# Performance work log

Measured on AMD Instinct MI355X. Metric: run time of the kernel, lower is better.

## Reference

```python
import jax, jax.numpy as jnp
import numpy as np

GAMMA = 1.0
BIG = 1e8  # boundary value used by the original numba kernel


def setup_inputs() -> dict:
    key = jax.random.key(0)
    k1, k2 = jax.random.split(key)
    N, M, d = 4096, 4096, 64
    x = jax.random.normal(k1, (N, d), dtype=jnp.float32)
    y = jax.random.normal(k2, (M, d), dtype=jnp.float32)
    return {"x": x, "y": y}


def _soft_dtw(D, gamma):
    """Soft-DTW DP R[N,M] via anti-diagonal wavefront scan.

    Matches compute_softdtw: R padded with BIG, R[0,0]=0,
    R[i,j] = D[i-1,j-1] + softmin_gamma(R[i-1,j-1], R[i-1,j], R[i,j-1]).
    Diagonals are stored as length-(N+2) vectors indexed by i (j = k - i).
    """
    N, M = D.shape
    ii = jnp.arange(1, N + 1)          # cell row indices 1..N
    inf = jnp.full((N + 2,), BIG, D.dtype)
    r_km2 = inf.at[0].set(0.0)          # diagonal k=0: only R[0,0]=0
    r_km1 = inf                         # diagonal k=1: all boundary

    def step(carry, k):
        r_km2, r_km1 = carry
        j = k - ii                      # column index per row on this diagonal
        valid = (j >= 1) & (j <= M)
        r0 = -r_km2[ii - 1] / gamma     # R[i-1, j-1]
        r1 = -r_km1[ii - 1] / gamma     # R[i-1, j]
        r2 = -r_km1[ii] / gamma         # R[i,   j-1]
        rmax = jnp.maximum(jnp.maximum(r0, r1), r2)
        rsum = jnp.exp(r0 - rmax) + jnp.exp(r1 - rmax) + jnp.exp(r2 - rmax)
        softmin = -gamma * (jnp.log(rsum) + rmax)
        jc = jnp.clip(j - 1, 0, M - 1)
        d_diag = D[ii - 1, jc]          # D[i-1, j-1] along this diagonal
        val = jnp.where(valid, d_diag + softmin, BIG)
        r_k = inf.at[1:N + 1].set(val)
        return (r_km1, r_k), None

    ks = jnp.arange(2, N + M + 1)
    (_, r_last), _ = jax.lax.scan(step, (r_km2, r_km1), ks)
    return r_last[N]                    # R[N, M]


def reference(x, y):
    # squared-euclidean distance matrix: sum((x_i - y_j)^2)
    x2 = jnp.sum(x * x, axis=1)
    y2 = jnp.sum(y * y, axis=1)
    D = x2[:, None] + y2[None, :] - 2.0 * (x @ y.T)  # [N, M]
    N, M = D.shape
    r = _soft_dtw(D, GAMMA)
    return r / (N + M)                   # open_end=False path
```

## Files before the change

kernel.cpp:

```cpp
#include <hip/hip_runtime.h>
#include <hip/hip_fp16.h>

#define Nn 4096
#define Mm 4096
#define NB 64
#define CH 16
#define NCHUNK 260
#define NCHUNKP 262
#define HPITCH 4352
#define HOFF 64
#define LOG2E 1.4426950408889634f
#define LN2 0.6931471805599453f
#define BIGX (1 << 23)

typedef unsigned long long ull;

__device__ __forceinline__ float hw_exp2(float x) { return __builtin_amdgcn_exp2f(x); }
__device__ __forceinline__ float hw_log2(float x) { return __builtin_amdgcn_logf(x); }

__device__ __forceinline__ float dpp_shr1(float v) {
    int r = __builtin_amdgcn_update_dpp(0, __float_as_int(v), 0x138, 0xF, 0xF, false);
    return __int_as_float(r);
}
__device__ __forceinline__ int dpp_shr1_i(int v) {
    return __builtin_amdgcn_update_dpp(0, v, 0x138, 0xF, 0xF, false);
}
__device__ __forceinline__ float dpp_shl1(float v) {
    int r = __builtin_amdgcn_update_dpp(0, __float_as_int(v), 0x130, 0xF, 0xF, false);
    return __int_as_float(r);
}
__device__ __forceinline__ int dpp_shl1_i(int v) {
    return __builtin_amdgcn_update_dpp(0, v, 0x130, 0xF, 0xF, false);
}
__device__ __forceinline__ float half_lo(int w) {
    return __low2float(__builtin_bit_cast(__half2, w));
}
__device__ __forceinline__ float half_hi(int w) {
    return __high2float(__builtin_bit_cast(__half2, w));
}
__device__ __forceinline__ ull packmx(float m, int X) {
    return (ull)__float_as_uint(m) | ((ull)(unsigned)X << 32);
}

__global__ __launch_bounds__(256) void dist_kernel(const float* __restrict__ x,
                                                   const float* __restrict__ y,
                                                   __half* __restrict__ Dsk) {
    __shared__ float xs[64][65];
    __shared__ float ys[80][65];
    __shared__ float dt[64][81];
    __shared__ float x2s[64], y2s[80];
    const int b = blockIdx.y, tj = blockIdx.x, tid = threadIdx.x;

    const float4* x4 = (const float4*)(x + (size_t)b * 64 * 64);
#pragma unroll
    for (int i = 0; i < 4; ++i) {
        int idx = tid + i * 256;
        int r = idx >> 4, c = (idx & 15) * 4;
        float4 v = x4[idx];
        xs[r][c] = v.x; xs[r][c + 1] = v.y; xs[r][c + 2] = v.z; xs[r][c + 3] = v.w;
    }
#pragma unroll
    for (int i = 0; i < 5; ++i) {
        int idx = tid + i * 256;
        int r = idx >> 4, c = (idx & 15) * 4;
        int rowg = tj * 64 + r; if (rowg > Mm - 1) rowg = Mm - 1;
        float4 w = ((const float4*)(y + (size_t)rowg * 64))[c >> 2];
        ys[r][c] = w.x; ys[r][c + 1] = w.y; ys[r][c + 2] = w.z; ys[r][c + 3] = w.w;
    }
    __syncthreads();

    if (tid < 64) {
        float a = 0.f;
#pragma unroll 8
        for (int k = 0; k < 64; ++k) a += xs[tid][k] * xs[tid][k];
        x2s[tid] = a;
    } else if (tid < 144) {
        int r = tid - 64;
        float a = 0.f;
#pragma unroll 8
        for (int k = 0; k < 64; ++k) a += ys[r][k] * ys[r][k];
        y2s[r] = a;
    }
    __syncthreads();

    const int r0 = (tid >> 4) * 4, c0 = (tid & 15) * 5;
    float acc[4][5] = {{0.f}};
#pragma unroll 4
    for (int k = 0; k < 64; ++k) {
        float a0 = xs[r0][k], a1 = xs[r0 + 1][k], a2 = xs[r0 + 2][k], a3 = xs[r0 + 3][k];
#pragma unroll
        for (int j = 0; j < 5; ++j) {
            float bj = ys[c0 + j][k];
            acc[0][j] = fmaf(a0, bj, acc[0][j]);
            acc[1][j] = fmaf(a1, bj, acc[1][j]);
            acc[2][j] = fmaf(a2, bj, acc[2][j]);
            acc[3][j] = fmaf(a3, bj, acc[3][j]);
        }
    }
#pragma unroll
    for (int i = 0; i < 4; ++i)
#pragma unroll
        for (int j = 0; j < 5; ++j)
            dt[r0 + i][c0 + j] =
                (x2s[r0 + i] + y2s[c0 + j] - 2.0f * acc[i][j]) * LOG2E;
    __syncthreads();

    const int l = tid & 63, q = tid >> 6;
    const int ci = ((l + 15) >> 4) + q;
    const int jj0 = 16 * ci - l;
    int w[8];
#pragma unroll
    for (int i = 0; i < 8; ++i) {
        __half2 hh;
        hh.x = __float2half(dt[l][jj0 + 2 * i]);
        hh.y = __float2half(dt[l][jj0 + 2 * i + 1]);
        w[i] = __builtin_bit_cast(int, hh);
    }
    {
        __half* dst = Dsk + (((size_t)b * NCHUNKP + 4 * tj + ci) * 64 + l) * 16;
        int4* d4 = (int4*)dst;
        d4[0] = make_int4(w[0], w[1], w[2], w[3]);
        d4[1] = make_int4(w[4], w[5], w[6], w[7]);
    }
    if (tj == 0 && q == 0) {
        const int cif = l >> 4;
        int wf[8];
#pragma unroll
        for (int i = 0; i < 8; ++i) {
            int ja = 16 * cif - l + 2 * i;     if (ja < 0) ja = 0;
            int jb = 16 * cif - l + 2 * i + 1; if (jb < 0) jb = 0;
            __half2 hh;
            hh.x = __float2half(dt[l][ja]);
            hh.y = __float2half(dt[l][jb]);
            wf[i] = __builtin_bit_cast(int, hh);
        }
        __half* dst = Dsk + (((size_t)b * NCHUNKP + cif) * 64 + l) * 16;
        int4* d4 = (int4*)dst;
        d4[0] = make_int4(wf[0], wf[1], wf[2], wf[3]);
        d4[1] = make_int4(wf[4], wf[5], wf[6], wf[7]);
    }
}

#define PREP(KM, NI, DV) \
    float dv_##KM = (DV); float nf_##KM = __builtin_rintf(dv_##KM); \
    int NI = (int)nf_##KM; float KM = hw_exp2(nf_##KM - dv_##KM);

#define STEP(KM, NI, IDX) do {                                                \
    float shufM = dpp_shr1(lM);                                               \
    int   shufX = dpp_shr1_i(lX);                                             \
    float upM = isL0 ? hRotM : shufM;                                         \
    int   upX = isL0 ? hRotX : shufX;                                         \
    float dgM = isL0 ? hPrevM : psM;                                          \
    int   dgX = isL0 ? hPrevX : psX;                                          \
    hPrevM = hRotM; hPrevX = hRotX;                                           \
    hRotM = dpp_shl1(hRotM); hRotX = dpp_shl1_i(hRotX);                       \
    int Xm = min(min(dgX, upX), lX);                                          \
    float ssum = ldexpf(dgM, Xm - dgX) + ldexpf(upM, Xm - upX) +              \
                 ldexpf(lM, Xm - lX);                                         \
    float mraw = ssum * (KM);                                                 \
    unsigned mb = __float_as_uint(mraw);                                      \
    int e = (int)((mb >> 23) & 0xFFu) - 126;                                  \
    psM = shufM; psX = shufX;                                                 \
    lM = __uint_as_float((mb & 0x807FFFFFu) | 0x3F000000u);                   \
    lX = Xm + (NI) - e;                                                       \
    if (doStore)                                                              \
        __hip_atomic_store(&HoutB[16 * c + (IDX) - 62], packmx(lM, lX),       \
                           __ATOMIC_RELAXED, __HIP_MEMORY_SCOPE_AGENT);       \
} while (0)

__global__ __launch_bounds__(64, 1) void dp_kernel(const __half* __restrict__ Dsk,
                                                   ull* __restrict__ H,
                                                   float* __restrict__ out) {
    const int l = threadIdx.x;
    const int b = blockIdx.x;
    const bool isL0 = (l == 0), isL63 = (l == 63), lastBand = (b == NB - 1);
    const int lt = l & 15;
    const __half* __restrict__ Db = Dsk + ((size_t)b * NCHUNKP * 64 + l) * 16;
    const ull* __restrict__ HinB = H + (size_t)b * HPITCH + HOFF;
    ull* __restrict__ HoutB = H + (size_t)(b + 1) * HPITCH + HOFF;
    const bool doH = (b > 0);
    const bool doStore = (!lastBand) && isL63;

    float lM = 0.5f;  int lX = BIGX;
    float psM = 0.5f; int psX = BIGX;
    float hPrevM = 0.5f; int hPrevX = (b == 0) ? -1 : BIGX;
    float hRotM; int hRotX;
    ull hNextU, hLoadU;
    int4 dn1A, dn1B, dn2A, dn2B;
    float rTM = 0.5f; int rTX = 0;

    {
        const int4* p = (const int4*)Db;
        dn1A = p[0]; dn1B = p[1];
        const int4* q = (const int4*)(Db + 1024);
        dn2A = q[0]; dn2B = q[1];
    }
    if (doH) {
        hNextU = __hip_atomic_load(&HinB[1 + lt],      __ATOMIC_RELAXED, __HIP_MEMORY_SCOPE_AGENT);
        hLoadU = __hip_atomic_load(&HinB[CH + 1 + lt], __ATOMIC_RELAXED, __HIP_MEMORY_SCOPE_AGENT);
    } else {
        hNextU = packmx(0.5f, BIGX);
        hLoadU = packmx(0.5f, BIGX);
    }

    for (int c = 0; c < NCHUNK; ++c) {
        int4 dcA = dn1A, dcB = dn1B;
        dn1A = dn2A; dn1B = dn2B;
        {
            const int4* p = (const int4*)(Db + (size_t)(c + 2) * 1024);
            dn2A = p[0]; dn2B = p[1];
        }
        hRotM = __uint_as_float((unsigned)hNextU);
        hRotX = (int)(unsigned)(hNextU >> 32);
        hNextU = hLoadU;
        if (doH && (c + 2 <= 255))
            hLoadU = __hip_atomic_load(&HinB[16 * (c + 2) + 1 + lt],
                                       __ATOMIC_RELAXED, __HIP_MEMORY_SCOPE_AGENT);
        if (doH && (c <= 255)) {
            while (__ballot(!(hRotM > 0.f))) {
                __builtin_amdgcn_s_sleep(1);
                ull v = __hip_atomic_load(&HinB[16 * c + 1 + lt],
                                          __ATOMIC_RELAXED, __HIP_MEMORY_SCOPE_AGENT);
                hRotM = __uint_as_float((unsigned)v);
                hRotX = (int)(unsigned)(v >> 32);
            }
        }

        PREP(k0,  n0,  half_lo(dcA.x)); PREP(k1,  n1,  half_hi(dcA.x));
        PREP(k2,  n2,  half_lo(dcA.y)); PREP(k3,  n3,  half_hi(dcA.y));
        PREP(k4,  n4,  half_lo(dcA.z)); PREP(k5,  n5,  half_hi(dcA.z));
        PREP(k6,  n6,  half_lo(dcA.w)); PREP(k7,  n7,  half_hi(dcA.w));
        PREP(k8,  n8,  half_lo(dcB.x)); PREP(k9,  n9,  half_hi(dcB.x));
        PREP(k10, n10, half_lo(dcB.y)); PREP(k11, n11, half_hi(dcB.y));
        PREP(k12, n12, half_lo(dcB.z)); PREP(k13, n13, half_hi(dcB.z));
        PREP(k14, n14, half_lo(dcB.w)); PREP(k15, n15, half_hi(dcB.w));

        STEP(k0,  n0,  0);  STEP(k1,  n1,  1);  STEP(k2,  n2,  2);
        STEP(k3,  n3,  3);  STEP(k4,  n4,  4);  STEP(k5,  n5,  5);
        STEP(k6,  n6,  6);  STEP(k7,  n7,  7);  STEP(k8,  n8,  8);
        STEP(k9,  n9,  9);  STEP(k10, n10, 10); STEP(k11, n11, 11);
        STEP(k12, n12, 12); STEP(k13, n13, 13); STEP(k14, n14, 14);
        if (c == NCHUNK - 1) { rTM = lM; rTX = lX; }
        STEP(k15, n15, 15);
    }

    if (lastBand && isL63) {
        float rpr = (float)rTX - hw_log2(rTM);
        out[0] = rpr * (LN2 / (float)(Nn + Mm));
    }
}

extern "C" void kernel_launch(void* const* d_in, const int* in_sizes, int n_in,
                              void* d_out, int out_size, void* d_ws, size_t ws_size,
                              hipStream_t stream) {
    const float* x = (const float*)d_in[0];
    const float* y = (const float*)d_in[1];
    float* out = (float*)d_out;

    char* ws = (char*)d_ws;
    __half* Dsk = (__half*)ws;
    size_t dskBytes = (size_t)NB * NCHUNKP * 64 * 16 * sizeof(__half);
    ull* H = (ull*)(ws + dskBytes);

    dist_kernel<<<dim3(64, 64), 256, 0, stream>>>(x, y, Dsk);
    dp_kernel<<<NB, 64, 0, stream>>>(Dsk, H, out);
}
```

Baseline: 1.215 ms.

## Group four DP bands per workgroup and hand off boundaries through an LDS ring

The soft-DTW wavefront DP previously ran one 64-lane band per block, with every band handing its boundary to the next through global memory and agent-scope polling. Now four bands run as four wavefronts in one 256-thread block. Neighbouring waves exchange boundary values through a shared-memory ring buffer with workgroup-scope atomics and a consumed counter for back-pressure. Only the block-to-block handoff still goes through global memory, and it adds a deeper four-entry prefetch and an initial wait for a few chunks to be ready. This is meant to cut the latency of inter-band communication, at the cost of more complex flow control and a possible deadlock if the ring credit logic is wrong.

```diff
diff --git a/kernel.cpp b/kernel.cpp
--- a/kernel.cpp
+++ b/kernel.cpp
@@ -4,6 +4,9 @@
 #define Nn 4096
 #define Mm 4096
 #define NB 64
+#define NWB 4
+#define NGB 16
+#define RING 16
 #define CH 16
 #define NCHUNK 260
 #define NCHUNKP 262
@@ -41,6 +44,8 @@
 __device__ __forceinline__ ull packmx(float m, int X) {
     return (ull)__float_as_uint(m) | ((ull)(unsigned)X << 32);
 }
+__device__ __forceinline__ float mxlo(ull v) { return __uint_as_float((unsigned)v); }
+__device__ __forceinline__ int   mxhi(ull v) { return (int)(unsigned)(v >> 32); }
 
 __global__ __launch_bounds__(256) void dist_kernel(const float* __restrict__ x,
                                                    const float* __restrict__ y,
@@ -163,31 +168,60 @@
     psM = shufM; psX = shufX;                                                 \
     lM = __uint_as_float((mb & 0x807FFFFFu) | 0x3F000000u);                   \
     lX = Xm + (NI) - e;                                                       \
-    if (doStore)                                                              \
-        __hip_atomic_store(&HoutB[16 * c + (IDX) - 62], packmx(lM, lX),       \
-                           __ATOMIC_RELAXED, __HIP_MEMORY_SCOPE_AGENT);       \
+    if (isL63) {                                                              \
+        if (prodG) {                                                          \
+            __hip_atomic_store(&HoutG[16 * c + (IDX) - 62], packmx(lM, lX),   \
+                               __ATOMIC_RELAXED, __HIP_MEMORY_SCOPE_AGENT);   \
+        } else if (prodL) {                                                   \
+            if ((IDX) < 15) {                                                 \
+                if (stA)                                                      \
+                    __hip_atomic_store(&rpA[(IDX) + 1], packmx(lM, lX),       \
+                                       __ATOMIC_RELAXED,                      \
+                                       __HIP_MEMORY_SCOPE_WORKGROUP);         \
+            } else {                                                          \
+                if (stB)                                                      \
+                    __hip_atomic_store(&rpB[0], packmx(lM, lX),               \
+                                       __ATOMIC_RELAXED,                      \
+                                       __HIP_MEMORY_SCOPE_WORKGROUP);         \
+            }                                                                 \
+        }                                                                     \
+    }                                                                         \
 } while (0)
 
-__global__ __launch_bounds__(64, 1) void dp_kernel(const __half* __restrict__ Dsk,
-                                                   ull* __restrict__ H,
-                                                   float* __restrict__ out) {
-    const int l = threadIdx.x;
-    const int b = blockIdx.x;
-    const bool isL0 = (l == 0), isL63 = (l == 63), lastBand = (b == NB - 1);
-    const int lt = l & 15;
-    const __half* __restrict__ Db = Dsk + ((size_t)b * NCHUNKP * 64 + l) * 16;
-    const ull* __restrict__ HinB = H + (size_t)b * HPITCH + HOFF;
-    ull* __restrict__ HoutB = H + (size_t)(b + 1) * HPITCH + HOFF;
-    const bool doH = (b > 0);
-    const bool doStore = (!lastBand) && isL63;
+__global__ __launch_bounds__(256, 1) void dp_kernel(const __half* __restrict__ Dsk,
+                                                    ull* __restrict__ H,
+                                                    float* __restrict__ out) {
+    __shared__ ull ring[NWB - 1][RING][16];
+    __shared__ int cnt[(NWB - 1) * 32];
+
+    const int tid = threadIdx.x;
+    const int w = tid >> 6, l = tid & 63, lt = l & 15;
+    const int g = blockIdx.x;
+    const int B = g * NWB + w;
+    const bool isL0 = (l == 0), isL63 = (l == 63), lastBand = (B == NB - 1);
+    const bool consL = (w > 0);
+    const bool consG = (w == 0) && (g > 0);
+    const bool prodL = (w < NWB - 1);
+    const bool prodG = (w == NWB - 1) && (g < NGB - 1);
+
+    const __half* __restrict__ Db = Dsk + ((size_t)B * NCHUNKP * 64 + l) * 16;
+    const ull* __restrict__ HinG = H + (size_t)g * HPITCH + HOFF;
+    ull* __restrict__ HoutG = H + (size_t)(g + 1) * HPITCH + HOFF;
+
+    {
+        ull* rf = &ring[0][0][0];
+        for (int i = tid; i < (NWB - 1) * RING * 16; i += 256) rf[i] = packmx(-1.0f, 0);
+        if (tid < NWB - 1) cnt[tid * 32] = -1;
+    }
+    __syncthreads();
 
     float lM = 0.5f;  int lX = BIGX;
     float psM = 0.5f; int psX = BIGX;
-    float hPrevM = 0.5f; int hPrevX = (b == 0) ? -1 : BIGX;
-    float hRotM; int hRotX;
-    ull hNextU, hLoadU;
+    float hPrevM = 0.5f; int hPrevX = (B == 0) ? -1 : BIGX;
+    float rTM = 0.5f; int rTX = 0;
     int4 dn1A, dn1B, dn2A, dn2B;
-    float rTM = 0.5f; int rTX = 0;
+    ull h0U, h1U, h2U, h3U;
+    ull hNextU = packmx(-1.0f, 0);
 
     {
         const int4* p = (const int4*)Db;
@@ -195,13 +229,25 @@
         const int4* q = (const int4*)(Db + 1024);
         dn2A = q[0]; dn2B = q[1];
     }
-    if (doH) {
-        hNextU = __hip_atomic_load(&HinB[1 + lt],      __ATOMIC_RELAXED, __HIP_MEMORY_SCOPE_AGENT);
-        hLoadU = __hip_atomic_load(&HinB[CH + 1 + lt], __ATOMIC_RELAXED, __HIP_MEMORY_SCOPE_AGENT);
+
+    if (consG) {
+        ull pv = __hip_atomic_load(&HinG[16 * 6 + 1 + lt], __ATOMIC_RELAXED,
+                                   __HIP_MEMORY_SCOPE_AGENT);
+        while (__ballot(!(mxlo(pv) > 0.f))) {
+            __builtin_amdgcn_s_sleep(8);
+            pv = __hip_atomic_load(&HinG[16 * 6 + 1 + lt], __ATOMIC_RELAXED,
+                                   __HIP_MEMORY_SCOPE_AGENT);
+        }
+        h0U = __hip_atomic_load(&HinG[1 + lt],      __ATOMIC_RELAXED, __HIP_MEMORY_SCOPE_AGENT);
+        h1U = __hip_atomic_load(&HinG[17 + lt],     __ATOMIC_RELAXED, __HIP_MEMORY_SCOPE_AGENT);
+        h2U = __hip_atomic_load(&HinG[33 + lt],     __ATOMIC_RELAXED, __HIP_MEMORY_SCOPE_AGENT);
+        h3U = __hip_atomic_load(&HinG[49 + lt],     __ATOMIC_RELAXED, __HIP_MEMORY_SCOPE_AGENT);
     } else {
-        hNextU = packmx(0.5f, BIGX);
-        hLoadU = packmx(0.5f, BIGX);
-    }
+        h0U = h1U = h2U = h3U = packmx(0.5f, BIGX);
+    }
+    if (consL)
+        hNextU = __hip_atomic_load(&ring[w - 1][0][lt], __ATOMIC_RELAXED,
+                                   __HIP_MEMORY_SCOPE_WORKGROUP);
 
     for (int c = 0; c < NCHUNK; ++c) {
         int4 dcA = dn1A, dcB = dn1B;
@@ -210,21 +256,62 @@
             const int4* p = (const int4*)(Db + (size_t)(c + 2) * 1024);
             dn2A = p[0]; dn2B = p[1];
         }
-        hRotM = __uint_as_float((unsigned)hNextU);
-        hRotX = (int)(unsigned)(hNextU >> 32);
-        hNextU = hLoadU;
-        if (doH && (c + 2 <= 255))
-            hLoadU = __hip_atomic_load(&HinB[16 * (c + 2) + 1 + lt],
-                                       __ATOMIC_RELAXED, __HIP_MEMORY_SCOPE_AGENT);
-        if (doH && (c <= 255)) {
-            while (__ballot(!(hRotM > 0.f))) {
-                __builtin_amdgcn_s_sleep(1);
-                ull v = __hip_atomic_load(&HinB[16 * c + 1 + lt],
-                                          __ATOMIC_RELAXED, __HIP_MEMORY_SCOPE_AGENT);
-                hRotM = __uint_as_float((unsigned)v);
-                hRotX = (int)(unsigned)(v >> 32);
+
+        float hRotM = 0.5f; int hRotX = BIGX;
+        if (consL) {
+            if (c <= 255) {
+                ull v = hNextU;
+                float mM = mxlo(v);
+                while (__ballot(!(mM > 0.f))) {
+                    __builtin_amdgcn_s_sleep(1);
+                    v = __hip_atomic_load(&ring[w - 1][c & (RING - 1)][lt],
+                                          __ATOMIC_RELAXED, __HIP_MEMORY_SCOPE_WORKGROUP);
+                    mM = mxlo(v);
+                }
+                hRotM = mM; hRotX = mxhi(v);
+                if (l < 16)
+                    __hip_atomic_store(&ring[w - 1][c & (RING - 1)][l], packmx(-1.0f, 0),
+                                       __ATOMIC_RELAXED, __HIP_MEMORY_SCOPE_WORKGROUP);
+                asm volatile("s_waitcnt lgkmcnt(0)" ::: "memory");
+                if (l == 0)
+                    __hip_atomic_store(&cnt[(w - 1) * 32], c, __ATOMIC_RELAXED,
+                                       __HIP_MEMORY_SCOPE_WORKGROUP);
+                if (c < 255)
+                    hNextU = __hip_atomic_load(&ring[w - 1][(c + 1) & (RING - 1)][lt],
+                                               __ATOMIC_RELAXED, __HIP_MEMORY_SCOPE_WORKGROUP);
             }
-        }
+        } else if (consG) {
+            if (c <= 255) {
+                ull v = h0U;
+                float mM = mxlo(v);
+                while (__ballot(!(mM > 0.f))) {
+                    __builtin_amdgcn_s_sleep(4);
+                    v = __hip_atomic_load(&HinG[16 * c + 1 + lt], __ATOMIC_RELAXED,
+                                          __HIP_MEMORY_SCOPE_AGENT);
+                    mM = mxlo(v);
+                }
+                hRotM = mM; hRotX = mxhi(v);
+                h0U = h1U; h1U = h2U; h2U = h3U;
+                h3U = (c + 4 <= 255)
+                        ? __hip_atomic_load(&HinG[16 * (c + 4) + 1 + lt], __ATOMIC_RELAXED,
+                                            __HIP_MEMORY_SCOPE_AGENT)
+                        : packmx(0.5f, BIGX);
+            }
+        }
+
+        if (prodL) {
+            int consd = __hip_atomic_load(&cnt[w * 32], __ATOMIC_RELAXED,
+                                          __HIP_MEMORY_SCOPE_WORKGROUP);
+            while (consd < c - 18) {
+                __builtin_amdgcn_s_sleep(4);
+                consd = __hip_atomic_load(&cnt[w * 32], __ATOMIC_RELAXED,
+                                          __HIP_MEMORY_SCOPE_WORKGROUP);
+            }
+        }
+        ull* rpA = &ring[w < NWB - 1 ? w : 0][(c - 4) & (RING - 1)][0];
+        ull* rpB = &ring[w < NWB - 1 ? w : 0][(c - 3) & (RING - 1)][0];
+        const bool stA = (c >= 4);
+        const bool stB = (c >= 3);
 
         PREP(k0,  n0,  half_lo(dcA.x)); PREP(k1,  n1,  half_hi(dcA.x));
         PREP(k2,  n2,  half_lo(dcA.y)); PREP(k3,  n3,  half_hi(dcA.y));
@@ -263,5 +350,5 @@
     ull* H = (ull*)(ws + dskBytes);
 
     dist_kernel<<<dim3(64, 64), 256, 0, stream>>>(x, y, Dsk);
-    dp_kernel<<<NB, 64, 0, stream>>>(Dsk, H, out);
-}
+    dp_kernel<<<NGB, 256, 0, stream>>>(Dsk, H, out);
+}
```

Result: slower. 1.597 ms (+31.4%).
